# Kernel tuning notes

Measured on AMD Instinct MI355X. Metric: run time of the kernel, lower is better.

The kernel has to match this reference:

```python
import jax, jax.numpy as jnp
import numpy as np

B, S, D = 8, 512, 256          # batch, seq_len, input_depth
E, H = 8, 4                    # num_experts, num_heads
DK = DV = DO = 256             # total_key/value/output depth (per expert)
DH = DK // H                   # head dim = 64
SCALE = DH ** -0.5


def setup_inputs() -> dict:
    key = jax.random.key(0)
    ks = jax.random.split(key, 8)
    queries = jax.random.normal(ks[0], (B, S, D), jnp.float32)
    keys = jax.random.normal(ks[1], (B, S, D), jnp.float32)
    values = jax.random.normal(ks[2], (B, S, D), jnp.float32)
    mask = jax.random.randint(ks[3], (B, S, S), 0, 2).astype(bool)
    s = 0.05
    Wq = jax.random.normal(ks[4], (D, DK * E), jnp.float32) * s
    Wk = jax.random.normal(ks[5], (D, DK * E), jnp.float32) * s
    Wv = jax.random.normal(ks[6], (D, DV * E), jnp.float32) * s
    Wo = jax.random.normal(ks[7], (DV, DO * E), jnp.float32) * s
    return {"queries": queries, "keys": keys, "values": values, "mask": mask,
            "Wq": Wq, "Wk": Wk, "Wv": Wv, "Wo": Wo}


def _split_heads(x):
    # [B, S, E*H*DH] -> [B, E, H, S, DH]
    b, s, _ = x.shape
    return x.reshape(b, s, E, H, -1).transpose(0, 2, 3, 1, 4)


def reference(queries, keys, values, mask, Wq, Wk, Wv, Wo):
    q = _split_heads(queries @ Wq) * SCALE   # [B,E,H,S,DH]
    k = _split_heads(keys @ Wk)
    v = _split_heads(values @ Wv)
    logits = jnp.einsum('behqd,behkd->behqk', q, k)      # [B,E,H,S,S]
    m = mask[:, None, None].astype(jnp.float32)          # [B,1,1,S,S]
    logits = logits * (1.0 - m) + (-1e18) * m
    w = jax.nn.softmax(logits, axis=-1)
    ctx = jnp.einsum('behqk,behkd->behqd', w, v)         # [B,E,H,S,DH]
    # merge heads -> [B, S, E, H*DH]
    ctx = ctx.transpose(0, 3, 1, 2, 4).reshape(B, S, E, H * DH)
    # faithful quirk: Dense applied on rank-4 tensor -> [B,S,E,DO*E]
    return ctx @ Wo
```

## Files before the change

### kernel.cpp

```cpp
#include <hip/hip_runtime.h>
#include <stdint.h>


typedef __bf16 bf16x8 __attribute__((ext_vector_type(8)));
typedef float f32x4 __attribute__((ext_vector_type(4)));
typedef unsigned short u16x8 __attribute__((ext_vector_type(8)));
typedef unsigned short u16x4 __attribute__((ext_vector_type(4)));

#define MFMA16(a, b, c) __builtin_amdgcn_mfma_f32_16x16x32_bf16(a, b, c, 0, 0, 0)

__device__ __forceinline__ unsigned short bfc(float x) {
    __bf16 b = (__bf16)x;
    return __builtin_bit_cast(unsigned short, b);
}

__device__ __forceinline__ void gload16(const void* g, void* l) {
    __builtin_amdgcn_global_load_lds(
        (const __attribute__((address_space(1))) void*)g,
        (__attribute__((address_space(3))) void*)l, 16, 0, 0);
}

#define QSCALE 0.18033688011112042f
#define MASKVAL -28.853900817779268f

__global__ __launch_bounds__(256) void prep_kern(
        const float* __restrict__ q, const float* __restrict__ k,
        const float* __restrict__ v, const int* __restrict__ mask,
        const float* __restrict__ Wq, const float* __restrict__ Wk,
        const float* __restrict__ Wv, const float* __restrict__ Wo,
        unsigned short* __restrict__ qb, unsigned short* __restrict__ kb,
        unsigned short* __restrict__ vb, unsigned short* __restrict__ wt,
        uint32_t* __restrict__ maskbits) {
    __shared__ float tile[32][33];
    const int x = blockIdx.x, t = threadIdx.x;
    if (x < 3072) {
        int which = x >> 10;
        const float* s = (which == 0) ? q : (which == 1) ? k : v;
        unsigned short* o = (which == 0) ? qb : (which == 1) ? kb : vb;
        int i = ((x & 1023) * 256 + t) * 4;
        float4 f = *(const float4*)&s[i];
        u16x4 r;
        r[0] = bfc(f.x); r[1] = bfc(f.y); r[2] = bfc(f.z); r[3] = bfc(f.w);
        *(u16x4*)&o[i] = r;
    } else if (x < 5120) {
        int y = x - 3072;
        int wsel = y >> 9;
        const float* W = (wsel == 0) ? Wq : (wsel == 1) ? Wk : (wsel == 2) ? Wv : Wo;
        unsigned short* T = wt + wsel * 2048 * 256;
        int rem = y & 511;
        int c0 = (rem & 63) * 32, r0 = (rem >> 6) * 32;
        int tr = t >> 3, tc = (t & 7) * 4;
        float4 f = *(const float4*)&W[(r0 + tr) * 2048 + c0 + tc];
        tile[tr][tc + 0] = f.x; tile[tr][tc + 1] = f.y;
        tile[tr][tc + 2] = f.z; tile[tr][tc + 3] = f.w;
        __syncthreads();
        u16x4 o;
        o[0] = bfc(tile[tc + 0][tr]); o[1] = bfc(tile[tc + 1][tr]);
        o[2] = bfc(tile[tc + 2][tr]); o[3] = bfc(tile[tc + 3][tr]);
        *(u16x4*)&T[(c0 + tr) * 256 + r0 + tc] = o;
    } else {
        const int lane = t & 63;
        int wi = ((x - 5120) * 4 + (t >> 6)) * 32;
        for (int i = 0; i < 32; ++i) {
            int u = wi + i;
            int b = u >> 12, rem = u & 4095, row = rem >> 3, ktp = rem & 7;
            int mv = mask[((size_t)(b * 512 + row)) * 512 + ktp * 64 + lane];
            unsigned long long bal = __ballot(mv != 0);
            if (lane == 0) {
                maskbits[(size_t)(b * 16 + ktp * 2) * 512 + row] = (uint32_t)bal;
                maskbits[(size_t)(b * 16 + ktp * 2 + 1) * 512 + row] = (uint32_t)(bal >> 32);
            }
        }
    }
}

__global__ __launch_bounds__(1024) void fused_kern(
        const unsigned short* __restrict__ actq,
        const unsigned short* __restrict__ actk,
        const unsigned short* __restrict__ actv,
        const unsigned short* __restrict__ Wt,
        const uint32_t* __restrict__ maskbits,
        unsigned short* __restrict__ CTX) {
    __shared__ unsigned short Klds[512 * 64];
    __shared__ unsigned short Vt[64 * 512];
    __shared__ unsigned short R3[64 * 128];
    const int bid = (int)blockIdx.x;
    const int flat = (bid & 7) * 32 + (bid >> 3);
    const int b = flat >> 5, eh = flat & 31;
    const int e = eh >> 2, h = eh & 3;
    const int t = threadIdx.x, w = t >> 6, l = t & 63, li = l & 15, g = l >> 4;
    const int tw0 = w * 32;
    const size_t actoff = (size_t)b * 512 * 256;
    const size_t wso = ((size_t)(e * 256 + h * 64)) * 256;

    bf16x8 qf[2][2];

    for (int p = 0; p < 3; ++p) {
        const unsigned short* A = ((p == 0) ? actq : (p == 1) ? actk : actv) + actoff;
        const unsigned short* W = Wt + (size_t)p * 2048 * 256 + wso;
        f32x4 acc[2][4];
#pragma unroll
        for (int m = 0; m < 2; ++m)
#pragma unroll
            for (int n = 0; n < 4; ++n) acc[m][n] = (f32x4){0.f, 0.f, 0.f, 0.f};
        for (int kh = 0; kh < 2; ++kh) {
            __syncthreads();
            {
                int nr = t >> 4, k8 = (t & 15) * 8;
                *(u16x8*)&R3[nr * 128 + (k8 ^ ((nr & 7) << 3))] =
                    *(const u16x8*)&W[(size_t)nr * 256 + kh * 128 + k8];
            }
            __syncthreads();
#pragma unroll
            for (int kk = 0; kk < 4; ++kk) {
                const int k0 = kh * 128 + kk * 32;
                bf16x8 af[2], bfr[4];
#pragma unroll
                for (int m = 0; m < 2; ++m)
                    af[m] = *(const bf16x8*)&A[(size_t)(tw0 + m * 16 + li) * 256 + k0 + g * 8];
#pragma unroll
                for (int n = 0; n < 4; ++n) {
                    int nr = n * 16 + li;
                    bfr[n] = *(const bf16x8*)&R3[nr * 128 + ((kk * 32 + g * 8) ^ ((nr & 7) << 3))];
                }
                if (p == 2) {
#pragma unroll
                    for (int m = 0; m < 2; ++m)
#pragma unroll
                        for (int n = 0; n < 4; ++n)
                            acc[m][n] = MFMA16(af[m], bfr[n], acc[m][n]);
                } else {
#pragma unroll
                    for (int m = 0; m < 2; ++m)
#pragma unroll
                        for (int n = 0; n < 4; ++n)
                            acc[m][n] = MFMA16(bfr[n], af[m], acc[m][n]);
                }
            }
        }
        if (p == 0) {
            unsigned short* qs = Klds + w * 2048;
#pragma unroll
            for (int m = 0; m < 2; ++m)
#pragma unroll
                for (int n = 0; n < 4; ++n) {
                    int row = m * 16 + li, dh = n * 16 + g * 4;
                    u16x4 o;
#pragma unroll
                    for (int i = 0; i < 4; ++i) o[i] = bfc(acc[m][n][i] * QSCALE);
                    *(u16x4*)&qs[row * 64 + (dh ^ ((row & 7) << 3))] = o;
                }
#pragma unroll
            for (int m = 0; m < 2; ++m) {
                int row = m * 16 + li;
                qf[m][0] = *(const bf16x8*)&qs[row * 64 + ((g * 8) ^ ((row & 7) << 3))];
                qf[m][1] = *(const bf16x8*)&qs[row * 64 + ((32 + g * 8) ^ ((row & 7) << 3))];
            }
        } else if (p == 1) {
#pragma unroll
            for (int m = 0; m < 2; ++m)
#pragma unroll
                for (int n = 0; n < 4; ++n) {
                    int tok = tw0 + m * 16 + li, dh = n * 16 + g * 4;
                    u16x4 o;
#pragma unroll
                    for (int i = 0; i < 4; ++i) o[i] = bfc(acc[m][n][i]);
                    *(u16x4*)&Klds[tok * 64 + (dh ^ (((tok >> 1) & 7) << 3))] = o;
                }
        } else {
#pragma unroll
            for (int m = 0; m < 2; ++m)
#pragma unroll
                for (int n = 0; n < 4; ++n) {
                    int tok = tw0 + m * 16 + g * 4, dh = n * 16 + li;
                    u16x4 o;
#pragma unroll
                    for (int i = 0; i < 4; ++i) o[i] = bfc(acc[m][n][i]);
                    *(u16x4*)&Vt[dh * 512 + (tok ^ ((dh & 7) << 3))] = o;
                }
        }
    }
    __syncthreads();

    bf16x8 vaug;
#pragma unroll
    for (int j = 0; j < 8; ++j) vaug[j] = (li == 0) ? (__bf16)1.0f : (__bf16)0.0f;
    f32x4 atc[2][4], lacc[2];
#pragma unroll
    for (int m = 0; m < 2; ++m) {
#pragma unroll
        for (int c = 0; c < 4; ++c) atc[m][c] = (f32x4){0.f, 0.f, 0.f, 0.f};
        lacc[m] = (f32x4){0.f, 0.f, 0.f, 0.f};
    }
    unsigned short* Pw = R3 + w * 512;
    const uint32_t* mb = maskbits + (size_t)b * 16 * 512;

    for (int kt = 0; kt < 16; ++kt) {
        bf16x8 kf[2][2];
#pragma unroll
        for (int f = 0; f < 2; ++f) {
            int tok = kt * 32 + 2 * li + f;
            const unsigned short* kr = &Klds[tok * 64];
            int sw = ((tok >> 1) & 7) << 3;
            kf[f][0] = *(const bf16x8*)&kr[(g * 8) ^ sw];
            kf[f][1] = *(const bf16x8*)&kr[(32 + g * 8) ^ sw];
        }
        f32x4 s[2][2];
#pragma unroll
        for (int m = 0; m < 2; ++m)
#pragma unroll
            for (int f = 0; f < 2; ++f) {
                f32x4 zz = (f32x4){0.f, 0.f, 0.f, 0.f};
                zz = MFMA16(qf[m][0], kf[f][0], zz);
                zz = MFMA16(qf[m][1], kf[f][1], zz);
                s[m][f] = zz;
            }
#pragma unroll
        for (int m = 0; m < 2; ++m) {
            const uint4 mw = *(const uint4*)&mb[(size_t)kt * 512 +
                                                tw0 + m * 16 + g * 4];
#pragma unroll
            for (int i = 0; i < 4; ++i) {
                uint32_t word = (i == 0) ? mw.x : (i == 1) ? mw.y : (i == 2) ? mw.z : mw.w;
                uint32_t pair = (word >> (2 * li)) & 3u;
                if (pair & 1u) s[m][0][i] = MASKVAL;
                if (pair & 2u) s[m][1][i] = MASKVAL;
            }
        }
        bf16x8 bv[4];
#pragma unroll
        for (int c = 0; c < 4; ++c) {
            int dh = c * 16 + li;
            bv[c] = *(const bf16x8*)&Vt[dh * 512 + ((kt * 32 + g * 8) ^ ((dh & 7) << 3))];
        }
#pragma unroll
        for (int m = 0; m < 2; ++m) {
#pragma unroll
            for (int i = 0; i < 4; ++i) {
                int row = g * 4 + i;
                uint32_t pk = (uint32_t)bfc(__builtin_exp2f(s[m][0][i])) |
                              ((uint32_t)bfc(__builtin_exp2f(s[m][1][i])) << 16);
                *(uint32_t*)&Pw[row * 32 + ((2 * li) ^ ((row & 3) << 3))] = pk;
            }
            bf16x8 pa = *(const bf16x8*)&Pw[li * 32 + ((g * 8) ^ ((li & 3) << 3))];
#pragma unroll
            for (int c = 0; c < 4; ++c)
                atc[m][c] = MFMA16(bv[c], pa, atc[m][c]);
            lacc[m] = MFMA16(vaug, pa, lacc[m]);
        }
    }
#pragma unroll
    for (int m = 0; m < 2; ++m) {
        float l_i = __shfl(lacc[m][0], l & 15, 64);
        float inv = 1.0f / l_i;
        const int qrow = tw0 + m * 16 + li;
#pragma unroll
        for (int c = 0; c < 4; ++c) {
            u16x4 o;
#pragma unroll
            for (int i = 0; i < 4; ++i) o[i] = bfc(atc[m][c][i] * inv);
            *(u16x4*)&CTX[(size_t)((b * 512 + qrow) * 8 + e) * 256 +
                          h * 64 + c * 16 + g * 4] = o;
        }
    }
}

__global__ __launch_bounds__(256) void gemm_kern(
        const unsigned short* __restrict__ A,
        const unsigned short* __restrict__ Bt,
        float* __restrict__ C, int cpx) {
    __shared__ __align__(16) unsigned char smem[32768];
    unsigned short* Asl = (unsigned short*)smem;
    unsigned short* Bsl = (unsigned short*)(smem + 16384);
    const int bid = (int)blockIdx.x;
    const int logical = (bid & 7) * cpx + (bid >> 3);
    const int bx = logical & 15;
    const int by = logical >> 4;
    const int t = threadIdx.x, l = t & 63, w = t >> 6;
    const int li = l & 15, g = l >> 4;
    const int wr = w >> 1, wc = w & 1;
    const int rowA = by * 128, colB = bx * 128;
    f32x4 acc[4][4];
#pragma unroll
    for (int m = 0; m < 4; ++m)
#pragma unroll
        for (int n = 0; n < 4; ++n) acc[m][n] = (f32x4){0.f, 0.f, 0.f, 0.f};

    for (int kk = 0; kk < 4; ++kk) {
#pragma unroll
        for (int j = 0; j < 4; ++j) {
            const int seg = j * 4 + w;
            const int chunk = seg * 64 + l;
            const int row = chunk >> 3, c8 = chunk & 7;
            const int src8 = (c8 ^ (row & 7)) * 8;
            gload16(&A[(size_t)(rowA + row) * 256 + kk * 64 + src8],
                    &Asl[seg * 512]);
            gload16(&Bt[(size_t)(colB + row) * 256 + kk * 64 + src8],
                    &Bsl[seg * 512]);
        }
        __syncthreads();
#pragma unroll
        for (int hh = 0; hh < 2; ++hh) {
            bf16x8 af[4], bfr[4];
#pragma unroll
            for (int m = 0; m < 4; ++m) {
                int row = wr * 64 + m * 16 + li;
                af[m] = *(const bf16x8*)&Asl[row * 64 + (((hh * 4 + g) ^ (row & 7)) * 8)];
            }
#pragma unroll
            for (int n = 0; n < 4; ++n) {
                int row = wc * 64 + n * 16 + li;
                bfr[n] = *(const bf16x8*)&Bsl[row * 64 + (((hh * 4 + g) ^ (row & 7)) * 8)];
            }
#pragma unroll
            for (int m = 0; m < 4; ++m)
#pragma unroll
                for (int n = 0; n < 4; ++n)
                    acc[m][n] = MFMA16(bfr[n], af[m], acc[m][n]);
        }
        __syncthreads();
    }
    float* osl = (float*)smem;
    const int wb = w * 1088;
#pragma unroll
    for (int m = 0; m < 4; ++m) {
#pragma unroll
        for (int n = 0; n < 4; ++n) {
            int c16 = (n * 4 + g) ^ (li & 3);
            *(f32x4*)&osl[wb + li * 68 + c16 * 4] = acc[m][n];
        }
#pragma unroll
        for (int r = 0; r < 4; ++r) {
            int chunk = r * 64 + l;
            int row = chunk >> 4, cic = chunk & 15;
            f32x4 v = *(const f32x4*)&osl[wb + row * 68 + (cic ^ (row & 3)) * 4];
            const int rr = rowA + wr * 64 + m * 16 + row;
            const int cc = colB + wc * 64 + cic * 4;
            __builtin_nontemporal_store(v, (f32x4*)&C[(size_t)rr * 2048 + cc]);
        }
    }
}

extern "C" void kernel_launch(void* const* d_in, const int* in_sizes, int n_in,
                              void* d_out, int out_size, void* d_ws, size_t ws_size,
                              hipStream_t stream) {
    (void)in_sizes; (void)n_in; (void)out_size; (void)ws_size;
    const float* queries = (const float*)d_in[0];
    const float* keys    = (const float*)d_in[1];
    const float* values  = (const float*)d_in[2];
    const int*   mask    = (const int*)d_in[3];
    const float* Wq = (const float*)d_in[4];
    const float* Wk = (const float*)d_in[5];
    const float* Wv = (const float*)d_in[6];
    const float* Wo = (const float*)d_in[7];

    unsigned short* CTX = (unsigned short*)d_ws;
    unsigned short* Qbf = CTX + (size_t)32768 * 256;
    unsigned short* Wt  = Qbf + (size_t)3 * 4096 * 256;
    uint32_t* maskbits  = (uint32_t*)(Wt + (size_t)4 * 2048 * 256);

    prep_kern<<<dim3(5376), 256, 0, stream>>>(queries, keys, values, mask,
                                              Wq, Wk, Wv, Wo,
                                              Qbf, Qbf + 4096 * 256, Qbf + 2 * 4096 * 256,
                                              Wt, maskbits);
    fused_kern<<<dim3(256), 1024, 0, stream>>>(Qbf, Qbf + 4096 * 256,
                                               Qbf + 2 * 4096 * 256,
                                               Wt, maskbits, CTX);
    gemm_kern<<<dim3(4096), 256, 0, stream>>>(CTX, Wt + (size_t)3 * 2048 * 256,
                                              (float*)d_out, 512);
}
```

Measured before the change: 140.2 us.

## Enlarge output GEMM tiles to 256x256 with double-buffered LDS staging

The output projection GEMM moves from 128x128 tiles with 256 threads to 256x256 tiles with 512 threads (8 waves, each computing 128x64). The K loop now double-buffers A and B in a 128KB LDS region, issuing the next stage's global-to-LDS loads before computing the current one. The goal is to cut redundant reloads of A and B and to overlap load latency with MFMA work. In exchange, each block uses far more LDS, which likely limits each CU to one block and reduces latency hiding for the large fp32 output stores.

```diff
diff --git a/kernel.cpp b/kernel.cpp
--- a/kernel.cpp
+++ b/kernel.cpp
@@ -265,65 +265,69 @@
     }
 }
 
-__global__ __launch_bounds__(256) void gemm_kern(
+__global__ __launch_bounds__(512, 2) void gemm_kern(
         const unsigned short* __restrict__ A,
         const unsigned short* __restrict__ Bt,
-        float* __restrict__ C, int cpx) {
-    __shared__ __align__(16) unsigned char smem[32768];
-    unsigned short* Asl = (unsigned short*)smem;
-    unsigned short* Bsl = (unsigned short*)(smem + 16384);
+        float* __restrict__ C) {
+    __shared__ __align__(16) unsigned char smem[131072];
     const int bid = (int)blockIdx.x;
-    const int logical = (bid & 7) * cpx + (bid >> 3);
-    const int bx = logical & 15;
-    const int by = logical >> 4;
+    const int logical = (bid & 7) * 128 + (bid >> 3);
+    const int bx = logical & 7;
+    const int by = logical >> 3;
     const int t = threadIdx.x, l = t & 63, w = t >> 6;
     const int li = l & 15, g = l >> 4;
-    const int wr = w >> 1, wc = w & 1;
-    const int rowA = by * 128, colB = bx * 128;
-    f32x4 acc[4][4];
-#pragma unroll
-    for (int m = 0; m < 4; ++m)
+    const int wr = w >> 2, wcn = w & 3;
+    const int rowA = by * 256, colB = bx * 256;
+
+    f32x4 acc[8][4];
+#pragma unroll
+    for (int m = 0; m < 8; ++m)
 #pragma unroll
         for (int n = 0; n < 4; ++n) acc[m][n] = (f32x4){0.f, 0.f, 0.f, 0.f};
 
-    for (int kk = 0; kk < 4; ++kk) {
+    auto STAGE = [&](int kk, int bsel) {
+        unsigned short* Ad = (unsigned short*)smem + bsel * 32768;
+        unsigned short* Bd = Ad + 16384;
 #pragma unroll
         for (int j = 0; j < 4; ++j) {
-            const int seg = j * 4 + w;
+            const int seg = j * 8 + w;
             const int chunk = seg * 64 + l;
             const int row = chunk >> 3, c8 = chunk & 7;
             const int src8 = (c8 ^ (row & 7)) * 8;
-            gload16(&A[(size_t)(rowA + row) * 256 + kk * 64 + src8],
-                    &Asl[seg * 512]);
-            gload16(&Bt[(size_t)(colB + row) * 256 + kk * 64 + src8],
-                    &Bsl[seg * 512]);
-        }
-        __syncthreads();
+            gload16(&A[(size_t)(rowA + row) * 256 + kk * 64 + src8], &Ad[seg * 512]);
+            gload16(&Bt[(size_t)(colB + row) * 256 + kk * 64 + src8], &Bd[seg * 512]);
+        }
+    };
+
+    STAGE(0, 0);
+    __syncthreads();
+    for (int kk = 0; kk < 4; ++kk) {
+        if (kk < 3) STAGE(kk + 1, (kk + 1) & 1);
+        const unsigned short* Ad = (const unsigned short*)smem + (kk & 1) * 32768;
+        const unsigned short* Bd = Ad + 16384;
 #pragma unroll
         for (int hh = 0; hh < 2; ++hh) {
-            bf16x8 af[4], bfr[4];
-#pragma unroll
-            for (int m = 0; m < 4; ++m) {
-                int row = wr * 64 + m * 16 + li;
-                af[m] = *(const bf16x8*)&Asl[row * 64 + (((hh * 4 + g) ^ (row & 7)) * 8)];
-            }
+            bf16x8 bfr[4];
 #pragma unroll
             for (int n = 0; n < 4; ++n) {
-                int row = wc * 64 + n * 16 + li;
-                bfr[n] = *(const bf16x8*)&Bsl[row * 64 + (((hh * 4 + g) ^ (row & 7)) * 8)];
-            }
-#pragma unroll
-            for (int m = 0; m < 4; ++m)
+                int c = wcn * 64 + n * 16 + li;
+                bfr[n] = *(const bf16x8*)&Bd[c * 64 + (((hh * 4 + g) ^ (c & 7)) * 8)];
+            }
+#pragma unroll
+            for (int m = 0; m < 8; ++m) {
+                int r = wr * 128 + m * 16 + li;
+                bf16x8 af = *(const bf16x8*)&Ad[r * 64 + (((hh * 4 + g) ^ (r & 7)) * 8)];
 #pragma unroll
                 for (int n = 0; n < 4; ++n)
-                    acc[m][n] = MFMA16(bfr[n], af[m], acc[m][n]);
+                    acc[m][n] = MFMA16(bfr[n], af, acc[m][n]);
+            }
         }
         __syncthreads();
     }
     float* osl = (float*)smem;
     const int wb = w * 1088;
 #pragma unroll
-    for (int m = 0; m < 4; ++m) {
+    for (int m = 0; m < 8; ++m) {
 #pragma unroll
         for (int n = 0; n < 4; ++n) {
             int c16 = (n * 4 + g) ^ (li & 3);
@@ -334,8 +338,8 @@
             int chunk = r * 64 + l;
             int row = chunk >> 4, cic = chunk & 15;
             f32x4 v = *(const f32x4*)&osl[wb + row * 68 + (cic ^ (row & 3)) * 4];
-            const int rr = rowA + wr * 64 + m * 16 + row;
-            const int cc = colB + wc * 64 + cic * 4;
+            const int rr = rowA + wr * 128 + m * 16 + row;
+            const int cc = colB + wcn * 64 + cic * 4;
             __builtin_nontemporal_store(v, (f32x4*)&C[(size_t)rr * 2048 + cc]);
         }
     }
@@ -366,6 +370,6 @@
     fused_kern<<<dim3(256), 1024, 0, stream>>>(Qbf, Qbf + 4096 * 256,
                                                Qbf + 2 * 4096 * 256,
                                                Wt, maskbits, CTX);
-    gemm_kern<<<dim3(4096), 256, 0, stream>>>(CTX, Wt + (size_t)3 * 2048 * 256,
-                                              (float*)d_out, 512);
-}
+    gemm_kern<<<dim3(1024), 512, 0, stream>>>(CTX, Wt + (size_t)3 * 2048 * 256,
+                                              (float*)d_out);
+}
```

Result: slower. 143.6 us (+2.4%).
